# Optimization experiments

Hardware: AMD Instinct MI355X
Metric: run time of the kernel (lower is better)

Reference implementation:

```python
import jax, jax.numpy as jnp
import numpy as np

B, N, D, H = 2, 2048, 1024, 16
HD = D // H
SCALE = HD ** -0.5

def setup_inputs() -> dict:
    key = jax.random.key(0)
    ks = jax.random.split(key, 5)
    x = jax.random.normal(ks[0], (B, N, D), dtype=jnp.float32)
    w_qkv = jax.random.normal(ks[1], (D, 3 * D), dtype=jnp.float32) * (1.0 / np.sqrt(D))
    b_qkv = jnp.zeros((3 * D,), dtype=jnp.float32)
    w_proj = jax.random.normal(ks[2], (D, D), dtype=jnp.float32) * (1.0 / np.sqrt(D))
    b_proj = jnp.zeros((D,), dtype=jnp.float32)
    return {"x": x, "w_qkv": w_qkv, "b_qkv": b_qkv, "w_proj": w_proj, "b_proj": b_proj}

def reference(x, w_qkv, b_qkv, w_proj, b_proj):
    # qkv projection: [B,N,3D] -> [3,B,H,N,HD]
    qkv = (x @ w_qkv + b_qkv).reshape(B, N, 3, H, HD).transpose(2, 0, 3, 1, 4)
    q, k, v = qkv[0], qkv[1], qkv[2]
    attn = jnp.einsum('bhnd,bhmd->bhnm', q, k) * SCALE  # [B,H,N,N]
    attn = jax.nn.softmax(attn, axis=-1)
    out = jnp.einsum('bhnm,bhmd->bhnd', attn, v)  # [B,H,N,HD]
    out = out.transpose(0, 2, 1, 3).reshape(B, N, D)
    return out @ w_proj + b_proj
```

## Files before the change

### kernel.cpp

```cpp
#include <hip/hip_runtime.h>
#include <cmath>

constexpr int Bb  = 2;
constexpr int Nn  = 2048;
constexpr int Dd  = 1024;
constexpr int Hh  = 16;
constexpr int HDd = 64;

#define QSCALE 0.18033688011112042f

typedef __attribute__((ext_vector_type(8))) _Float16 f16x8;
typedef __attribute__((ext_vector_type(2))) __fp16   fp16x2;
typedef __attribute__((ext_vector_type(4))) float    f32x4;

__device__ inline unsigned short f2h(float f) {
  _Float16 h = (_Float16)f;
  union { _Float16 h; unsigned short u; } v; v.h = h; return v.u;
}
__device__ inline unsigned cvt_pk_f16(float x, float y) {
  union { fp16x2 h; unsigned u; } v;
  v.h = __builtin_amdgcn_cvt_pkrtz(x, y);
  return v.u;
}
__device__ inline float fexp2(float x) {
  float r;
  asm("v_exp_f32 %0, %1" : "=v"(r) : "v"(x));
  return r;
}
__device__ inline void gload16(const void* g, void* l) {
  __builtin_amdgcn_global_load_lds((const __attribute__((address_space(1))) void*)g,
                                   (__attribute__((address_space(3))) void*)l, 16, 0, 0);
}

__global__ __launch_bounds__(256) void prep(
    const float* __restrict__ X, const float* __restrict__ Wq,
    const float* __restrict__ Wp,
    unsigned short* __restrict__ Xf, unsigned short* __restrict__ Bqt,
    unsigned short* __restrict__ Bpt)
{
  const int bid = blockIdx.x;
  const int t = threadIdx.x;

  if (bid < 2048) {
    const size_t i = ((size_t)bid * 256 + t) * 8;
    float4 u0 = *(const float4*)(X + i);
    float4 u1 = *(const float4*)(X + i + 4);
    ushort4 a, b;
    a.x = f2h(u0.x); a.y = f2h(u0.y); a.z = f2h(u0.z); a.w = f2h(u0.w);
    b.x = f2h(u1.x); b.y = f2h(u1.y); b.z = f2h(u1.z); b.w = f2h(u1.w);
    *(ushort4*)(Xf + i)     = a;
    *(ushort4*)(Xf + i + 4) = b;
    return;
  }

  __shared__ float T[64][65];
  const float* W; unsigned short* Wt; int Nd, n0, k0;
  if (bid < 2816) {
    const int b2 = bid - 2048;
    W = Wq; Wt = Bqt; Nd = 3 * Dd;
    n0 = (b2 % 48) * 64; k0 = (b2 / 48) * 64;
  } else {
    const int b3 = bid - 2816;
    W = Wp; Wt = Bpt; Nd = Dd;
    n0 = (b3 & 15) * 64; k0 = (b3 >> 4) * 64;
  }
  const int Kd = Dd;
#pragma unroll
  for (int i = 0; i < 4; ++i) {
    int idx = t + 256 * i;
    int r = idx >> 4, c4 = (idx & 15) * 4;
    float4 v = *(const float4*)(W + (size_t)(k0 + r) * Nd + n0 + c4);
    T[c4 + 0][r] = v.x; T[c4 + 1][r] = v.y;
    T[c4 + 2][r] = v.z; T[c4 + 3][r] = v.w;
  }
  __syncthreads();
#pragma unroll
  for (int i = 0; i < 4; ++i) {
    int idx = t + 256 * i;
    int nr = idx >> 4, kc = (idx & 15) * 4;
    ushort4 hv;
    hv.x = f2h(T[nr][kc + 0]); hv.y = f2h(T[nr][kc + 1]);
    hv.z = f2h(T[nr][kc + 2]); hv.w = f2h(T[nr][kc + 3]);
    *(ushort4*)(Wt + (size_t)(n0 + nr) * Kd + k0 + kc) = hv;
  }
}

template<int EPI>
__global__ __launch_bounds__(256, 4) void gemm_f16(
    const unsigned short* __restrict__ Ag,
    const unsigned short* __restrict__ Bg,
    const float* __restrict__ bias,
    float* __restrict__ Cout,
    unsigned short* __restrict__ Qf, unsigned short* __restrict__ Kf,
    unsigned short* __restrict__ Vtf,
    int Nsz, int Ksz, int gridM)
{
  __shared__ __align__(16) unsigned short A_s[8192];
  __shared__ __align__(16) unsigned short B_s[8192];

  const int t    = threadIdx.x;
  const int lane = t & 63, w = t >> 6;
  const int g = lane >> 4, lid = lane & 15;
  const int wr = w >> 1, wc = w & 1;

  const int nwg = gridDim.x;
  const int per = nwg >> 3;
  const int bid = (blockIdx.x & 7) * per + (blockIdx.x >> 3);
  const int by = bid % gridM, bx = bid / gridM;
  const int row0 = by * 128, col0 = bx * 128;

  f32x4 acc[4][4];
#pragma unroll
  for (int i = 0; i < 4; ++i)
#pragma unroll
    for (int j = 0; j < 4; ++j) acc[i][j] = f32x4{0.f, 0.f, 0.f, 0.f};

  const int sg8 = ((lane & 7) ^ (lane >> 3)) * 8;
  const int rl8 = lane >> 3;

  for (int k0 = 0; k0 < Ksz; k0 += 64) {
#pragma unroll
    for (int q = 0; q < 4; ++q) {
      const int oct = w * 4 + q;
      const int r = oct * 8 + rl8;
      gload16(Ag + (size_t)(row0 + r) * Ksz + k0 + sg8, A_s + oct * 512);
      gload16(Bg + (size_t)(col0 + r) * Ksz + k0 + sg8, B_s + oct * 512);
    }
    __syncthreads();

#pragma unroll
    for (int kk = 0; kk < 2; ++kk) {
      f16x8 a[4], b[4];
#pragma unroll
      for (int mb = 0; mb < 4; ++mb) {
        const int r = wr * 64 + mb * 16 + lid;
        const int off = r * 64 + (((kk * 4 + g) ^ (r & 7)) << 3);
        a[mb] = *(const f16x8*)(A_s + off);
      }
#pragma unroll
      for (int nb = 0; nb < 4; ++nb) {
        const int c = wc * 64 + nb * 16 + lid;
        const int off = c * 64 + (((kk * 4 + g) ^ (c & 7)) << 3);
        b[nb] = *(const f16x8*)(B_s + off);
      }
#pragma unroll
      for (int mb = 0; mb < 4; ++mb)
#pragma unroll
        for (int nb = 0; nb < 4; ++nb)
          acc[mb][nb] = __builtin_amdgcn_mfma_f32_16x16x32_f16(a[mb], b[nb], acc[mb][nb], 0, 0, 0);
    }
    __syncthreads();
  }

#pragma unroll
  for (int nb = 0; nb < 4; ++nb) {
    const int cg = col0 + wc * 64 + nb * 16 + lid;
    const float bv = bias[cg];
    if (EPI == 0) {
#pragma unroll
      for (int mb = 0; mb < 4; ++mb)
#pragma unroll
        for (int reg = 0; reg < 4; ++reg) {
          int nrow = row0 + wr * 64 + mb * 16 + 4 * g + reg;
          Cout[(size_t)nrow * Nsz + cg] = acc[mb][nb][reg] + bv;
        }
    } else {
      const int region = cg >> 10;
      const int h  = (cg & 1023) >> 6;
      const int hd = cg & 63;
      const int b2 = row0 >> 11;
      const int bh_ = b2 * Hh + h;
      const float sc = (region == 0) ? QSCALE : 1.0f;
#pragma unroll
      for (int mb = 0; mb < 4; ++mb) {
        const int nt0 = (row0 & 2047) + wr * 64 + mb * 16 + 4 * g;
        float cc[4];
#pragma unroll
        for (int reg = 0; reg < 4; ++reg) cc[reg] = (acc[mb][nb][reg] + bv) * sc;
        if (region == 2) {
          ushort4 vv;
          vv.x = f2h(cc[0]); vv.y = f2h(cc[1]);
          vv.z = f2h(cc[2]); vv.w = f2h(cc[3]);
          *(ushort4*)(Vtf + ((size_t)bh_ * HDd + hd) * Nn + nt0) = vv;
        } else {
          unsigned short* P = (region == 0) ? Qf : Kf;
#pragma unroll
          for (int reg = 0; reg < 4; ++reg)
            P[((size_t)bh_ * Nn + nt0 + reg) * HDd + hd] = f2h(cc[reg]);
        }
      }
    }
  }
}

__global__ __launch_bounds__(512, 2) void attn_mfma(
    const unsigned short* __restrict__ Qf, const unsigned short* __restrict__ Kf,
    const unsigned short* __restrict__ Vt,
    unsigned short* __restrict__ Of)
{
  __shared__ __align__(16) unsigned short Kf_s[16384];
  __shared__ __align__(16) unsigned short Vt_s[16384];
  __shared__ __align__(16) unsigned short P_s[8][2][1024];

  const int t    = threadIdx.x;
  const int lane = t & 63, w = t >> 6;
  const int g    = lane >> 4, lid = lane & 15;

  const int hw = blockIdx.x;
  const int bh = (hw & 7) * 4 + ((hw >> 3) & 3);
  const int q0 = (hw >> 5) * 256;
  const int b_ = bh >> 4, h_ = bh & 15;

  const size_t kvbase = (size_t)bh * Nn * HDd;

  const int qrowA = q0 + w * 16 + lid;
  const unsigned short* qpA = Qf + kvbase + (size_t)qrowA * HDd + g * 8;
  f16x8 qa0 = *(const f16x8*)(qpA);
  f16x8 qa1 = *(const f16x8*)(qpA + 32);
  const unsigned short* qpB = qpA + (size_t)128 * HDd;
  f16x8 qb0 = *(const f16x8*)(qpB);
  f16x8 qb1 = *(const f16x8*)(qpB + 32);

  f16x8 vones;
#pragma unroll
  for (int i = 0; i < 8; ++i) vones[i] = (_Float16)1.0f;

  f32x4 oA[4], oB[4];
  f32x4 olA = f32x4{0.f, 0.f, 0.f, 0.f};
  f32x4 olB = f32x4{0.f, 0.f, 0.f, 0.f};
#pragma unroll
  for (int i = 0; i < 4; ++i) { oA[i] = f32x4{0.f,0.f,0.f,0.f}; oB[i] = f32x4{0.f,0.f,0.f,0.f}; }

  const int sg8 = ((lane & 7) ^ (lane >> 3)) * 8;
  const int rsw = (lid & 7) << 4;

  char* PbA = (char*)&P_s[w][0][0];
  char* PbB = (char*)&P_s[w][1][0];

  auto stage = [&](int buf, int kv0) {
#pragma unroll
    for (int q = 0; q < 4; ++q) {
      const int idx = w * 4 + q;
      if (idx < 16) {
        const int oct = idx;
        const int r = oct * 8 + (lane >> 3);
        gload16(Kf + kvbase + (size_t)(kv0 + r) * HDd + sg8,
                Kf_s + buf * 8192 + oct * 512);
      } else {
        const int qd = idx - 16;
        const int r = qd * 4 + (lane >> 4);
        const int srcc = (lane & 15) ^ (r & 15);
        gload16(Vt + kvbase + (size_t)r * Nn + kv0 + srcc * 8,
                Vt_s + buf * 8192 + qd * 512);
      }
    }
  };

  stage(0, 0);
  int cur = 0;
  const int NT = Nn / 128;

  for (int tt = 0; tt < NT; ++tt) {
    __syncthreads();
    if (tt + 1 < NT) stage(cur ^ 1, (tt + 1) * 128);

    const int kb = cur * 8192;

    f32x4 sA[8], sB[8];
#pragma unroll
    for (int jbb = 0; jbb < 8; ++jbb) { sA[jbb] = f32x4{0.f,0.f,0.f,0.f}; sB[jbb] = f32x4{0.f,0.f,0.f,0.f}; }
    __builtin_amdgcn_s_setprio(1);
#pragma unroll
    for (int jbb = 0; jbb < 8; ++jbb) {
      const int row = jbb * 16 + lid;
      const int rs = kb + row * 64;
      const int sw = row & 7;
      f16x8 kf0 = *(const f16x8*)&Kf_s[rs + ((g       ^ sw)) * 8];
      f16x8 kf1 = *(const f16x8*)&Kf_s[rs + (((4 + g) ^ sw)) * 8];
      sA[jbb] = __builtin_amdgcn_mfma_f32_16x16x32_f16(kf0, qa0, sA[jbb], 0, 0, 0);
      sA[jbb] = __builtin_amdgcn_mfma_f32_16x16x32_f16(kf1, qa1, sA[jbb], 0, 0, 0);
      sB[jbb] = __builtin_amdgcn_mfma_f32_16x16x32_f16(kf0, qb0, sB[jbb], 0, 0, 0);
      sB[jbb] = __builtin_amdgcn_mfma_f32_16x16x32_f16(kf1, qb1, sB[jbb], 0, 0, 0);
    }
    __builtin_amdgcn_s_setprio(0);

#pragma unroll
    for (int jbb = 0; jbb < 8; ++jbb)
#pragma unroll
      for (int reg = 0; reg < 4; ++reg) {
        sA[jbb][reg] = fexp2(sA[jbb][reg]);
        sB[jbb][reg] = fexp2(sB[jbb][reg]);
      }

#pragma unroll
    for (int h = 0; h < 2; ++h) {
      const int wb = lid * 128;
#pragma unroll
      for (int jb = 0; jb < 4; ++jb) {
        const int jbb = h * 4 + jb;
        const int off = wb + ((32 * jb + 8 * g) ^ rsw);
        *(uint2*)(PbA + off) = make_uint2(cvt_pk_f16(sA[jbb][0], sA[jbb][1]),
                                          cvt_pk_f16(sA[jbb][2], sA[jbb][3]));
        *(uint2*)(PbB + off) = make_uint2(cvt_pk_f16(sB[jbb][0], sB[jbb][1]),
                                          cvt_pk_f16(sB[jbb][2], sB[jbb][3]));
      }
      __builtin_amdgcn_sched_barrier(0);

      const int rb = lid * 128;
      f16x8 pA0 = *(const f16x8*)(PbA + rb + ((16 * g) ^ rsw));
      f16x8 pA1 = *(const f16x8*)(PbA + rb + ((64 + 16 * g) ^ rsw));
      f16x8 pB0 = *(const f16x8*)(PbB + rb + ((16 * g) ^ rsw));
      f16x8 pB1 = *(const f16x8*)(PbB + rb + ((64 + 16 * g) ^ rsw));
      __builtin_amdgcn_s_setprio(1);
      olA = __builtin_amdgcn_mfma_f32_16x16x32_f16(pA0, vones, olA, 0, 0, 0);
      olA = __builtin_amdgcn_mfma_f32_16x16x32_f16(pA1, vones, olA, 0, 0, 0);
      olB = __builtin_amdgcn_mfma_f32_16x16x32_f16(pB0, vones, olB, 0, 0, 0);
      olB = __builtin_amdgcn_mfma_f32_16x16x32_f16(pB1, vones, olB, 0, 0, 0);
#pragma unroll
      for (int cb = 0; cb < 4; ++cb) {
        const int vrow = cb * 16 + lid;
        const int vs = kb + vrow * 128;
        const int sw = vrow & 15;
        f16x8 vb0 = *(const f16x8*)&Vt_s[vs + (((8 * h + g)     ^ sw)) * 8];
        f16x8 vb1 = *(const f16x8*)&Vt_s[vs + (((8 * h + 4 + g) ^ sw)) * 8];
        oA[cb] = __builtin_amdgcn_mfma_f32_16x16x32_f16(pA0, vb0, oA[cb], 0, 0, 0);
        oA[cb] = __builtin_amdgcn_mfma_f32_16x16x32_f16(pA1, vb1, oA[cb], 0, 0, 0);
        oB[cb] = __builtin_amdgcn_mfma_f32_16x16x32_f16(pB0, vb0, oB[cb], 0, 0, 0);
        oB[cb] = __builtin_amdgcn_mfma_f32_16x16x32_f16(pB1, vb1, oB[cb], 0, 0, 0);
      }
      __builtin_amdgcn_s_setprio(0);
      __builtin_amdgcn_sched_barrier(0);
    }
    cur ^= 1;
  }

  const size_t obaseA = ((size_t)(b_ * Nn + q0 + w * 16)) * Dd + h_ * 64;
  const size_t obaseB = obaseA + (size_t)128 * Dd;
#pragma unroll
  for (int reg = 0; reg < 4; ++reg) {
    const int row = 4 * g + reg;
    const float ivA = 1.0f / olA[reg];
    const float ivB = 1.0f / olB[reg];
#pragma unroll
    for (int cb = 0; cb < 4; ++cb) {
      Of[obaseA + (size_t)row * Dd + cb * 16 + lid] = f2h(oA[cb][reg] * ivA);
      Of[obaseB + (size_t)row * Dd + cb * 16 + lid] = f2h(oB[cb][reg] * ivB);
    }
  }
}

extern "C" void kernel_launch(void* const* d_in, const int* in_sizes, int n_in,
                              void* d_out, int out_size, void* d_ws, size_t ws_size,
                              hipStream_t stream)
{
  const float* x      = (const float*)d_in[0];
  const float* w_qkv  = (const float*)d_in[1];
  const float* b_qkv  = (const float*)d_in[2];
  const float* w_proj = (const float*)d_in[3];
  const float* b_proj = (const float*)d_in[4];
  float* outp = (float*)d_out;

  unsigned char* ws = (unsigned char*)d_ws;
  const size_t MB = 1ull << 20;
  unsigned short* Xf  = (unsigned short*)(ws +  0 * MB);
  unsigned short* Bqt = (unsigned short*)(ws +  8 * MB);
  unsigned short* Qf  = (unsigned short*)(ws + 14 * MB);
  unsigned short* Kf  = (unsigned short*)(ws + 22 * MB);
  unsigned short* Vtf = (unsigned short*)(ws + 30 * MB);
  unsigned short* Ofb = (unsigned short*)(ws + 38 * MB);
  unsigned short* Bpt = (unsigned short*)(ws + 46 * MB);

  const int M = Bb * Nn;

  prep<<<dim3(3072), 256, 0, stream>>>(x, w_qkv, w_proj, Xf, Bqt, Bpt);

  gemm_f16<1><<<dim3((3 * Dd / 128) * (M / 128)), 256, 0, stream>>>(
      Xf, Bqt, b_qkv, nullptr, Qf, Kf, Vtf, 3 * Dd, Dd, M / 128);

  attn_mfma<<<dim3((Nn / 256) * Bb * Hh), 512, 0, stream>>>(Qf, Kf, Vtf, Ofb);

  gemm_f16<0><<<dim3((Dd / 128) * (M / 128)), 256, 0, stream>>>(
      Ofb, Bpt, b_proj, outp, nullptr, nullptr, nullptr, Dd, Dd, M / 128);
}
```

Baseline: 104.0 us.

## Permute V layout to feed P directly from registers, shrink attention blocks

The QKV GEMM epilogue now writes V transposed with a permuted key order within each 32-key group. This lets the attention kernel pack exp'd scores straight from MFMA accumulator registers into the A operand of the PV MFMA, removing the per-warp LDS round trip for P. The attention block also drops from 512 to 256 threads covering 128 queries, which doubles the grid and frees the P shared buffer. Smaller blocks mean each block stages K/V for fewer queries, so K/V traffic per query rises in exchange for less LDS use and more blocks.

```diff
diff --git a/kernel.cpp b/kernel.cpp
--- a/kernel.cpp
+++ b/kernel.cpp
@@ -178,10 +178,11 @@
 #pragma unroll
         for (int reg = 0; reg < 4; ++reg) cc[reg] = (acc[mb][nb][reg] + bv) * sc;
         if (region == 2) {
+          const int ns = (nt0 & ~31) | ((nt0 & 12) << 1) | ((nt0 & 16) >> 2);
           ushort4 vv;
           vv.x = f2h(cc[0]); vv.y = f2h(cc[1]);
           vv.z = f2h(cc[2]); vv.w = f2h(cc[3]);
-          *(ushort4*)(Vtf + ((size_t)bh_ * HDd + hd) * Nn + nt0) = vv;
+          *(ushort4*)(Vtf + ((size_t)bh_ * HDd + hd) * Nn + ns) = vv;
         } else {
           unsigned short* P = (region == 0) ? Qf : Kf;
 #pragma unroll
@@ -193,14 +194,13 @@
   }
 }
 
-__global__ __launch_bounds__(512, 2) void attn_mfma(
+__global__ __launch_bounds__(256, 2) void attn_mfma(
     const unsigned short* __restrict__ Qf, const unsigned short* __restrict__ Kf,
     const unsigned short* __restrict__ Vt,
     unsigned short* __restrict__ Of)
 {
   __shared__ __align__(16) unsigned short Kf_s[16384];
   __shared__ __align__(16) unsigned short Vt_s[16384];
-  __shared__ __align__(16) unsigned short P_s[8][2][1024];
 
   const int t    = threadIdx.x;
   const int lane = t & 63, w = t >> 6;
@@ -208,7 +208,7 @@
 
   const int hw = blockIdx.x;
   const int bh = (hw & 7) * 4 + ((hw >> 3) & 3);
-  const int q0 = (hw >> 5) * 256;
+  const int q0 = (hw >> 5) * 128;
   const int b_ = bh >> 4, h_ = bh & 15;
 
   const size_t kvbase = (size_t)bh * Nn * HDd;
@@ -217,7 +217,7 @@
   const unsigned short* qpA = Qf + kvbase + (size_t)qrowA * HDd + g * 8;
   f16x8 qa0 = *(const f16x8*)(qpA);
   f16x8 qa1 = *(const f16x8*)(qpA + 32);
-  const unsigned short* qpB = qpA + (size_t)128 * HDd;
+  const unsigned short* qpB = qpA + (size_t)64 * HDd;
   f16x8 qb0 = *(const f16x8*)(qpB);
   f16x8 qb1 = *(const f16x8*)(qpB + 32);
 
@@ -232,20 +232,15 @@
   for (int i = 0; i < 4; ++i) { oA[i] = f32x4{0.f,0.f,0.f,0.f}; oB[i] = f32x4{0.f,0.f,0.f,0.f}; }
 
   const int sg8 = ((lane & 7) ^ (lane >> 3)) * 8;
-  const int rsw = (lid & 7) << 4;
-
-  char* PbA = (char*)&P_s[w][0][0];
-  char* PbB = (char*)&P_s[w][1][0];
 
   auto stage = [&](int buf, int kv0) {
 #pragma unroll
-    for (int q = 0; q < 4; ++q) {
-      const int idx = w * 4 + q;
+    for (int q = 0; q < 8; ++q) {
+      const int idx = w * 8 + q;
       if (idx < 16) {
-        const int oct = idx;
-        const int r = oct * 8 + (lane >> 3);
+        const int r = idx * 8 + (lane >> 3);
         gload16(Kf + kvbase + (size_t)(kv0 + r) * HDd + sg8,
-                Kf_s + buf * 8192 + oct * 512);
+                Kf_s + buf * 8192 + idx * 512);
       } else {
         const int qd = idx - 16;
         const int r = qd * 4 + (lane >> 4);
@@ -259,6 +254,8 @@
   stage(0, 0);
   int cur = 0;
   const int NT = Nn / 128;
+
+  union PU { unsigned u[4]; f16x8 v; };
 
   for (int tt = 0; tt < NT; ++tt) {
     __syncthreads();
@@ -285,37 +282,33 @@
     __builtin_amdgcn_s_setprio(0);
 
 #pragma unroll
-    for (int jbb = 0; jbb < 8; ++jbb)
-#pragma unroll
-      for (int reg = 0; reg < 4; ++reg) {
-        sA[jbb][reg] = fexp2(sA[jbb][reg]);
-        sB[jbb][reg] = fexp2(sB[jbb][reg]);
-      }
-
-#pragma unroll
     for (int h = 0; h < 2; ++h) {
-      const int wb = lid * 128;
-#pragma unroll
-      for (int jb = 0; jb < 4; ++jb) {
-        const int jbb = h * 4 + jb;
-        const int off = wb + ((32 * jb + 8 * g) ^ rsw);
-        *(uint2*)(PbA + off) = make_uint2(cvt_pk_f16(sA[jbb][0], sA[jbb][1]),
-                                          cvt_pk_f16(sA[jbb][2], sA[jbb][3]));
-        *(uint2*)(PbB + off) = make_uint2(cvt_pk_f16(sB[jbb][0], sB[jbb][1]),
-                                          cvt_pk_f16(sB[jbb][2], sB[jbb][3]));
-      }
-      __builtin_amdgcn_sched_barrier(0);
-
-      const int rb = lid * 128;
-      f16x8 pA0 = *(const f16x8*)(PbA + rb + ((16 * g) ^ rsw));
-      f16x8 pA1 = *(const f16x8*)(PbA + rb + ((64 + 16 * g) ^ rsw));
-      f16x8 pB0 = *(const f16x8*)(PbB + rb + ((16 * g) ^ rsw));
-      f16x8 pB1 = *(const f16x8*)(PbB + rb + ((64 + 16 * g) ^ rsw));
+#pragma unroll
+      for (int jb = 0; jb < 4; ++jb)
+#pragma unroll
+        for (int reg = 0; reg < 4; ++reg) {
+          sA[h * 4 + jb][reg] = fexp2(sA[h * 4 + jb][reg]);
+          sB[h * 4 + jb][reg] = fexp2(sB[h * 4 + jb][reg]);
+        }
+
+      PU pA0, pA1, pB0, pB1;
+#pragma unroll
+      for (int jb = 0; jb < 2; ++jb) {
+        pA0.u[2 * jb + 0] = cvt_pk_f16(sA[h * 4 + jb][0], sA[h * 4 + jb][1]);
+        pA0.u[2 * jb + 1] = cvt_pk_f16(sA[h * 4 + jb][2], sA[h * 4 + jb][3]);
+        pA1.u[2 * jb + 0] = cvt_pk_f16(sA[h * 4 + 2 + jb][0], sA[h * 4 + 2 + jb][1]);
+        pA1.u[2 * jb + 1] = cvt_pk_f16(sA[h * 4 + 2 + jb][2], sA[h * 4 + 2 + jb][3]);
+        pB0.u[2 * jb + 0] = cvt_pk_f16(sB[h * 4 + jb][0], sB[h * 4 + jb][1]);
+        pB0.u[2 * jb + 1] = cvt_pk_f16(sB[h * 4 + jb][2], sB[h * 4 + jb][3]);
+        pB1.u[2 * jb + 0] = cvt_pk_f16(sB[h * 4 + 2 + jb][0], sB[h * 4 + 2 + jb][1]);
+        pB1.u[2 * jb + 1] = cvt_pk_f16(sB[h * 4 + 2 + jb][2], sB[h * 4 + 2 + jb][3]);
+      }
+
       __builtin_amdgcn_s_setprio(1);
-      olA = __builtin_amdgcn_mfma_f32_16x16x32_f16(pA0, vones, olA, 0, 0, 0);
-      olA = __builtin_amdgcn_mfma_f32_16x16x32_f16(pA1, vones, olA, 0, 0, 0);
-      olB = __builtin_amdgcn_mfma_f32_16x16x32_f16(pB0, vones, olB, 0, 0, 0);
-      olB = __builtin_amdgcn_mfma_f32_16x16x32_f16(pB1, vones, olB, 0, 0, 0);
+      olA = __builtin_amdgcn_mfma_f32_16x16x32_f16(pA0.v, vones, olA, 0, 0, 0);
+      olA = __builtin_amdgcn_mfma_f32_16x16x32_f16(pA1.v, vones, olA, 0, 0, 0);
+      olB = __builtin_amdgcn_mfma_f32_16x16x32_f16(pB0.v, vones, olB, 0, 0, 0);
+      olB = __builtin_amdgcn_mfma_f32_16x16x32_f16(pB1.v, vones, olB, 0, 0, 0);
 #pragma unroll
       for (int cb = 0; cb < 4; ++cb) {
         const int vrow = cb * 16 + lid;
@@ -323,19 +316,18 @@
         const int sw = vrow & 15;
         f16x8 vb0 = *(const f16x8*)&Vt_s[vs + (((8 * h + g)     ^ sw)) * 8];
         f16x8 vb1 = *(const f16x8*)&Vt_s[vs + (((8 * h + 4 + g) ^ sw)) * 8];
-        oA[cb] = __builtin_amdgcn_mfma_f32_16x16x32_f16(pA0, vb0, oA[cb], 0, 0, 0);
-        oA[cb] = __builtin_amdgcn_mfma_f32_16x16x32_f16(pA1, vb1, oA[cb], 0, 0, 0);
-        oB[cb] = __builtin_amdgcn_mfma_f32_16x16x32_f16(pB0, vb0, oB[cb], 0, 0, 0);
-        oB[cb] = __builtin_amdgcn_mfma_f32_16x16x32_f16(pB1, vb1, oB[cb], 0, 0, 0);
+        oA[cb] = __builtin_amdgcn_mfma_f32_16x16x32_f16(pA0.v, vb0, oA[cb], 0, 0, 0);
+        oA[cb] = __builtin_amdgcn_mfma_f32_16x16x32_f16(pA1.v, vb1, oA[cb], 0, 0, 0);
+        oB[cb] = __builtin_amdgcn_mfma_f32_16x16x32_f16(pB0.v, vb0, oB[cb], 0, 0, 0);
+        oB[cb] = __builtin_amdgcn_mfma_f32_16x16x32_f16(pB1.v, vb1, oB[cb], 0, 0, 0);
       }
       __builtin_amdgcn_s_setprio(0);
-      __builtin_amdgcn_sched_barrier(0);
     }
     cur ^= 1;
   }
 
   const size_t obaseA = ((size_t)(b_ * Nn + q0 + w * 16)) * Dd + h_ * 64;
-  const size_t obaseB = obaseA + (size_t)128 * Dd;
+  const size_t obaseB = obaseA + (size_t)64 * Dd;
 #pragma unroll
   for (int reg = 0; reg < 4; ++reg) {
     const int row = 4 * g + reg;
@@ -377,7 +369,7 @@
   gemm_f16<1><<<dim3((3 * Dd / 128) * (M / 128)), 256, 0, stream>>>(
       Xf, Bqt, b_qkv, nullptr, Qf, Kf, Vtf, 3 * Dd, Dd, M / 128);
 
-  attn_mfma<<<dim3((Nn / 256) * Bb * Hh), 512, 0, stream>>>(Qf, Kf, Vtf, Ofb);
+  attn_mfma<<<dim3((Nn / 128) * Bb * Hh), 256, 0, stream>>>(Qf, Kf, Vtf, Ofb);
 
   gemm_f16<0><<<dim3((Dd / 128) * (M / 128)), 256, 0, stream>>>(
       Ofb, Bpt, b_proj, outp, nullptr, nullptr, nullptr, Dd, Dd, M / 128);
```

After: 103.1 us. No clear change (-0.9%).
